# Optimization experiments

Measured on AMD Instinct MI355X. Metric: run time of the kernel, lower is better.

The kernel has to match this reference:

```python
import jax, jax.numpy as jnp
import numpy as np

B, T, M, DK, DV, S = 64, 256, 64, 128, 256, 128
NSK, NQ = 200, 2000


def _glorot(k, shape):
    lim = np.sqrt(6.0 / (shape[0] + shape[1])).astype(np.float32)
    return jax.random.uniform(k, shape, jnp.float32, -lim, lim)


def setup_inputs() -> dict:
    key = jax.random.key(0)
    ks = jax.random.split(key, 16)
    tn = lambda k, shape: 0.1 * jax.random.truncated_normal(k, -2.0, 2.0, shape, jnp.float32)
    return {
        "q_data": jax.random.randint(ks[0], (B, T), 0, NSK + 1),
        "qa_data": jax.random.randint(ks[1], (B, T), 0, 2 * NSK + 1),
        "s_data": jax.random.randint(ks[2], (B, T), 0, NQ + 1),
        "key_memory": tn(ks[3], (M, DK)),
        "value_memory": tn(ks[4], (M, DV)),
        "Eq": 0.05 * jax.random.normal(ks[5], (NSK + 1, DK), jnp.float32),
        "Eqa": 0.05 * jax.random.normal(ks[6], (2 * NSK + 1, DV), jnp.float32),
        "Es": 0.05 * jax.random.normal(ks[7], (NQ + 1, DK), jnp.float32),
        "We": _glorot(ks[8], (DV, DV)), "be": jnp.zeros((DV,), jnp.float32),
        "Wa": _glorot(ks[9], (DV, DV)), "ba": jnp.zeros((DV,), jnp.float32),
        "Wsa": _glorot(ks[10], (DV, M)), "bsa": jnp.zeros((M,), jnp.float32),
        "Wqd1": _glorot(ks[11], (DK, S)), "bqd1": jnp.zeros((S,), jnp.float32),
        "Wqd": _glorot(ks[12], (S, 1)), "bqd": jnp.zeros((1,), jnp.float32),
        "Wsd1": _glorot(ks[13], (DK, S)), "bsd1": jnp.zeros((S,), jnp.float32),
        "Wsd": _glorot(ks[14], (S, 1)), "bsd": jnp.zeros((1,), jnp.float32),
    }


def reference(q_data, qa_data, s_data, key_memory, value_memory, Eq, Eqa, Es,
              We, be, Wa, ba, Wsa, bsa, Wqd1, bqd1, Wqd, bqd, Wsd1, bsd1, Wsd, bsd):
    b = q_data.shape[0]
    qe = Eq[q_data]    # [B,T,DK]
    qae = Eqa[qa_data]  # [B,T,DV]
    se = Es[s_data]    # [B,T,DK]
    # time-independent precomputation (same math, hoisted out of the loop)
    corr = jax.nn.softmax(jnp.einsum("btk,mk->btm", qe, key_memory), axis=-1)  # [B,T,M]
    erase = qae @ We + be  # [B,T,DV] (activation=None in source)
    add = qae @ Wa + ba    # [B,T,DV]
    qd = jnp.tanh(qe @ Wqd1 + bqd1) @ Wqd + bqd  # [B,T,1]
    sd = jnp.tanh(se @ Wsd1 + bsd1) @ Wsd + bsd  # [B,T,1]

    def step(Mv, x):
        cw, er, ad = x  # [B,M], [B,DV], [B,DV]
        read = jnp.einsum("bm,bmd->bd", cw, Mv)        # read BEFORE write
        sa1 = read @ Wsa + bsa                          # [B,M]
        sa = jnp.sum(cw * sa1, axis=1)                  # [B]
        scale = cw[:, :, None]                          # [B,M,1]
        Mv_new = Mv * (1.0 - er[:, None, :] * scale) + ad[:, None, :] * scale
        return Mv_new, sa

    Mv0 = jnp.broadcast_to(value_memory[None], (b,) + value_memory.shape)
    xs = (corr.transpose(1, 0, 2), erase.transpose(1, 0, 2), add.transpose(1, 0, 2))
    _, sa_t = jax.lax.scan(step, Mv0, xs)  # sa_t: [T,B]
    z = 3.0 * sa_t.T - qd[..., 0] - sd[..., 0]  # [B,T]
    return jax.nn.sigmoid(z)
```

## Files before the change

### kernel.cpp

```cpp
#include <hip/hip_runtime.h>
#include <math.h>

#define B_   64
#define T_   256
#define M_   64
#define DK_  128
#define DV_  256
#define S_   128
#define NQR  201
#define NQAR 401
#define NSR  2001

static __device__ __forceinline__ int imin(int a, int b){ return a < b ? a : b; }

static __device__ __forceinline__ float fast_tanh(float x){
  float e = __expf(2.f * x);
  return 1.f - 2.f / (e + 1.f);
}

template<int CTRL, int RM>
static __device__ __forceinline__ float dppadd(float x) {
  return x + __int_as_float(
      __builtin_amdgcn_update_dpp(0, __float_as_int(x), CTRL, RM, 0xf, true));
}
static __device__ __forceinline__ float wave_sum_lane63(float x) {
  x = dppadd<0x111, 0xf>(x);
  x = dppadd<0x112, 0xf>(x);
  x = dppadd<0x114, 0xf>(x);
  x = dppadd<0x118, 0xf>(x);
  x = dppadd<0x142, 0xa>(x);
  x = dppadd<0x143, 0xc>(x);
  return x;
}

__device__ void corr_role(int blk, const float* __restrict__ Eq,
                          const float* __restrict__ Km,
                          const float* __restrict__ Wsa,
                          const float* __restrict__ bsa,
                          float* __restrict__ corr,
                          float* __restrict__ w2_t,
                          float* __restrict__ csb_t)
{
  __shared__ float eq[4][DK_];
  __shared__ float cwb[4][M_];
  const int w = threadIdx.x >> 6, m = threadIdx.x & 63;
  const int i  = blk * 4 + w;
  const int ic = imin(i, NQR - 1);
  eq[w][m]      = Eq[ic * DK_ + m];
  eq[w][m + 64] = Eq[ic * DK_ + 64 + m];
  float acc = 0.f;
  const float4* kr = (const float4*)(Km + m * DK_);
  #pragma unroll 8
  for (int k4 = 0; k4 < DK_ / 4; ++k4) {
    float4 kv = kr[k4];
    acc = fmaf(eq[w][k4 * 4 + 0], kv.x, acc);
    acc = fmaf(eq[w][k4 * 4 + 1], kv.y, acc);
    acc = fmaf(eq[w][k4 * 4 + 2], kv.z, acc);
    acc = fmaf(eq[w][k4 * 4 + 3], kv.w, acc);
  }
  float mx = acc;
  #pragma unroll
  for (int off = 32; off; off >>= 1) mx = fmaxf(mx, __shfl_xor(mx, off, 64));
  float e = __expf(acc - mx);
  float ssum = e;
  #pragma unroll
  for (int off = 32; off; off >>= 1) ssum += __shfl_xor(ssum, off, 64);
  const float cw = e / ssum;
  if (i < NQR) corr[i * M_ + m] = cw;
  cwb[w][m] = cw;

  float pv = wave_sum_lane63(cw * bsa[m]);
  if (m == 63 && i < NQR) csb_t[i] = pv;

  float aw[4] = {0,0,0,0};
  for (int mm = 0; mm < M_; ++mm) {
    const float c = cwb[w][mm];
    #pragma unroll
    for (int r = 0; r < 4; ++r)
      aw[r] = fmaf(c, Wsa[(r * 64 + m) * M_ + mm], aw[r]);
  }
  if (i < NQR) {
    #pragma unroll
    for (int r = 0; r < 4; ++r) w2_t[i * DV_ + r * 64 + m] = aw[r];
  }
}

__device__ void ea_role(int blk, const float* __restrict__ Eqa,
                        const float* __restrict__ We, const float* __restrict__ be,
                        const float* __restrict__ Wa, const float* __restrict__ ba,
                        float* __restrict__ ert, float* __restrict__ adt)
{
  __shared__ float a[8][DV_];
  const int d  = threadIdx.x;
  const int i0 = blk * 8;
  #pragma unroll
  for (int r = 0; r < 8; ++r) a[r][d] = Eqa[imin(i0 + r, NQAR - 1) * DV_ + d];
  __syncthreads();
  float er[8] = {0,0,0,0,0,0,0,0}, ad[8] = {0,0,0,0,0,0,0,0};
  for (int k = 0; k < DV_; ++k) {
    float we = We[k * DV_ + d];
    float wa = Wa[k * DV_ + d];
    #pragma unroll
    for (int r = 0; r < 8; ++r) {
      er[r] = fmaf(a[r][k], we, er[r]);
      ad[r] = fmaf(a[r][k], wa, ad[r]);
    }
  }
  const float beo = be[d], bao = ba[d];
  #pragma unroll
  for (int r = 0; r < 8; ++r) {
    int i = i0 + r;
    if (i < NQAR) { ert[i * DV_ + d] = er[r] + beo; adt[i * DV_ + d] = ad[r] + bao; }
  }
}

__device__ void mlp_role(int blk, const float* __restrict__ E,
                         const float* __restrict__ W1, const float* __restrict__ b1,
                         const float* __restrict__ W2v, const float* __restrict__ b2,
                         float* __restrict__ outt, int nrows)
{
  __shared__ float e[8 * S_];
  __shared__ float red[8][2];
  const int tid = threadIdx.x;
  const int s = tid & 127, rh = tid >> 7;
  const int i0 = blk * 8;
  #pragma unroll
  for (int j = 0; j < 4; ++j) {
    int x = tid + j * 256;
    int row = imin(i0 + (x >> 7), nrows - 1);
    e[x] = E[row * DK_ + (x & 127)];
  }
  __syncthreads();
  float acc[4] = {0,0,0,0};
  const float* eb = e + rh * 4 * 128;
  for (int k = 0; k < DK_; ++k) {
    float wv = W1[k * S_ + s];
    #pragma unroll
    for (int r = 0; r < 4; ++r) acc[r] = fmaf(eb[r * 128 + k], wv, acc[r]);
  }
  const float b1s = b1[s], w2s = W2v[s];
  float p[4];
  #pragma unroll
  for (int r = 0; r < 4; ++r) p[r] = fast_tanh(acc[r] + b1s) * w2s;
  #pragma unroll
  for (int r = 0; r < 4; ++r) p[r] = wave_sum_lane63(p[r]);
  const int lane = tid & 63;
  const int half = s >> 6;
  if (lane == 63) {
    #pragma unroll
    for (int r = 0; r < 4; ++r) red[rh * 4 + r][half] = p[r];
  }
  __syncthreads();
  if (tid < 8) {
    int i = i0 + tid;
    if (i < nrows) outt[i] = red[tid][0] + red[tid][1] + b2[0];
  }
}

#define NB_CORR 51
#define NB_EA   51
#define NB_QD   26
#define NB_SD   251
#define NB_TOT  (NB_CORR + NB_EA + NB_QD + NB_SD)

__global__ __launch_bounds__(256) void tables_kernel(
    const float* Eq, const float* Km, const float* Wsa, const float* bsa,
    float* corr_t, float* w2_t, float* csb_t,
    const float* Eqa, const float* We, const float* be,
    const float* Wa, const float* ba, float* er_t, float* ad_t,
    const float* Wqd1, const float* bqd1, const float* Wqd, const float* bqd, float* qd_t,
    const float* Es, const float* Wsd1, const float* bsd1, const float* Wsd, const float* bsd, float* sd_t)
{
  int blk = blockIdx.x;
  if (blk < NB_CORR) { corr_role(blk, Eq, Km, Wsa, bsa, corr_t, w2_t, csb_t); return; }
  blk -= NB_CORR;
  if (blk < NB_EA)   { ea_role(blk, Eqa, We, be, Wa, ba, er_t, ad_t); return; }
  blk -= NB_EA;
  if (blk < NB_QD)   { mlp_role(blk, Eq, Wqd1, bqd1, Wqd, bqd, qd_t, NQR); return; }
  blk -= NB_QD;
  mlp_role(blk, Es, Wsd1, bsd1, Wsd, bsd, sd_t, NSR);
}

struct SOps { float4 c; float er, ad, w2; };

static __device__ __forceinline__ void fetch4(
    int ii, const int4& qq, const int4& qaq, int m0, int d,
    const float* __restrict__ corr_t, const float* __restrict__ er_t,
    const float* __restrict__ ad_t, const float* __restrict__ w2_t,
    SOps (&o)[4])
{
  const int q0 = __builtin_amdgcn_readlane(qq.x,  ii);
  const int q1 = __builtin_amdgcn_readlane(qq.y,  ii);
  const int q2 = __builtin_amdgcn_readlane(qq.z,  ii);
  const int q3 = __builtin_amdgcn_readlane(qq.w,  ii);
  const int a0 = __builtin_amdgcn_readlane(qaq.x, ii);
  const int a1 = __builtin_amdgcn_readlane(qaq.y, ii);
  const int a2 = __builtin_amdgcn_readlane(qaq.z, ii);
  const int a3 = __builtin_amdgcn_readlane(qaq.w, ii);
  o[0].c = *(const float4*)(corr_t + q0 * M_ + m0);
  o[1].c = *(const float4*)(corr_t + q1 * M_ + m0);
  o[2].c = *(const float4*)(corr_t + q2 * M_ + m0);
  o[3].c = *(const float4*)(corr_t + q3 * M_ + m0);
  o[0].er = er_t[a0 * DV_ + d];  o[0].ad = ad_t[a0 * DV_ + d];  o[0].w2 = w2_t[q0 * DV_ + d];
  o[1].er = er_t[a1 * DV_ + d];  o[1].ad = ad_t[a1 * DV_ + d];  o[1].w2 = w2_t[q1 * DV_ + d];
  o[2].er = er_t[a2 * DV_ + d];  o[2].ad = ad_t[a2 * DV_ + d];  o[2].w2 = w2_t[q2 * DV_ + d];
  o[3].er = er_t[a3 * DV_ + d];  o[3].ad = ad_t[a3 * DV_ + d];  o[3].w2 = w2_t[q3 * DV_ + d];
}

static __device__ __forceinline__ float step1(float (&Mv)[4], const SOps& o)
{
  float r0 = Mv[0] * o.c.x;
  float r1 = Mv[1] * o.c.y;
  r0 = fmaf(Mv[2], o.c.z, r0);
  r1 = fmaf(Mv[3], o.c.w, r1);
  Mv[0] = fmaf(o.c.x, fmaf(-o.er, Mv[0], o.ad), Mv[0]);
  Mv[1] = fmaf(o.c.y, fmaf(-o.er, Mv[1], o.ad), Mv[1]);
  Mv[2] = fmaf(o.c.z, fmaf(-o.er, Mv[2], o.ad), Mv[2]);
  Mv[3] = fmaf(o.c.w, fmaf(-o.er, Mv[3], o.ad), Mv[3]);
  return wave_sum_lane63((r0 + r1) * o.w2);
}

__global__ __launch_bounds__(512) void scan_kernel(
    const int* __restrict__ q_data, const int* __restrict__ qa_data,
    const float* __restrict__ corr_t, const float* __restrict__ er_t,
    const float* __restrict__ ad_t, const float* __restrict__ w2_t,
    const float* __restrict__ Vm, float* __restrict__ sa_part)
{
  const int b  = blockIdx.y;
  const int xx = blockIdx.x;
  const int dq = xx >> 1;
  const int mh = xx & 1;
  const int tid = threadIdx.x;
  const int dl  = tid & 63;
  const int w   = tid >> 6;
  const int mg  = mh * 8 + w;
  const int m0  = __builtin_amdgcn_readfirstlane(mg * 4);
  const int d   = dq * 64 + dl;

  const int4 qq  = ((const int4*)(q_data  + b * T_))[dl];
  const int4 qaq = ((const int4*)(qa_data + b * T_))[dl];

  float Mv[4];
  #pragma unroll
  for (int j = 0; j < 4; ++j) Mv[j] = Vm[(m0 + j) * DV_ + d];

  float* baseP = sa_part + ((dq * 16 + mg) * B_ + b) * T_;

  SOps A[4], B[4];
  fetch4(0, qq, qaq, m0, d, corr_t, er_t, ad_t, w2_t, A);
  fetch4(1, qq, qaq, m0, d, corr_t, er_t, ad_t, w2_t, B);

  for (int i = 0; i < 64; i += 2) {
    float4 pA;
    pA.x = step1(Mv, A[0]);
    pA.y = step1(Mv, A[1]);
    pA.z = step1(Mv, A[2]);
    pA.w = step1(Mv, A[3]);
    fetch4((i + 2) & 63, qq, qaq, m0, d, corr_t, er_t, ad_t, w2_t, A);
    if (dl == 63) *(float4*)(baseP + 4 * i) = pA;

    float4 pB;
    pB.x = step1(Mv, B[0]);
    pB.y = step1(Mv, B[1]);
    pB.z = step1(Mv, B[2]);
    pB.w = step1(Mv, B[3]);
    fetch4((i + 3) & 63, qq, qaq, m0, d, corr_t, er_t, ad_t, w2_t, B);
    if (dl == 63) *(float4*)(baseP + 4 * i + 4) = pB;
  }
}

__global__ __launch_bounds__(256) void final_kernel(
    const int* __restrict__ q_data, const int* __restrict__ s_data,
    const float* __restrict__ sa_part, const float* __restrict__ csb_t,
    const float* __restrict__ qd_t, const float* __restrict__ sd_t,
    float* __restrict__ out)
{
  const int b = blockIdx.x, t = threadIdx.x;
  float s = 0.f;
  #pragma unroll
  for (int p = 0; p < 64; ++p) s += sa_part[(p * B_ + b) * T_ + t];
  const int bt = b * T_ + t;
  const int q  = q_data[bt];
  const int si = s_data[bt];
  const float sa = s + csb_t[q];
  const float z = 3.f * sa - qd_t[q] - sd_t[si];
  out[bt] = 1.f / (1.f + __expf(-z));
}

extern "C" void kernel_launch(void* const* d_in, const int* in_sizes, int n_in,
                              void* d_out, int out_size, void* d_ws, size_t ws_size,
                              hipStream_t stream)
{
  const int*   q_data = (const int*)d_in[0];
  const int*   qa_data= (const int*)d_in[1];
  const int*   s_data = (const int*)d_in[2];
  const float* Km     = (const float*)d_in[3];
  const float* Vm     = (const float*)d_in[4];
  const float* Eq     = (const float*)d_in[5];
  const float* Eqa    = (const float*)d_in[6];
  const float* Es     = (const float*)d_in[7];
  const float* We     = (const float*)d_in[8];
  const float* be     = (const float*)d_in[9];
  const float* Wa     = (const float*)d_in[10];
  const float* ba     = (const float*)d_in[11];
  const float* Wsa    = (const float*)d_in[12];
  const float* bsa    = (const float*)d_in[13];
  const float* Wqd1   = (const float*)d_in[14];
  const float* bqd1   = (const float*)d_in[15];
  const float* Wqd    = (const float*)d_in[16];
  const float* bqd    = (const float*)d_in[17];
  const float* Wsd1   = (const float*)d_in[18];
  const float* bsd1   = (const float*)d_in[19];
  const float* Wsd    = (const float*)d_in[20];
  const float* bsd    = (const float*)d_in[21];
  float* out = (float*)d_out;

  float* wsf    = (float*)d_ws;
  float* corr_t = wsf;
  float* w2_t   = corr_t + NQR * M_;
  float* csb_t  = w2_t + NQR * DV_;
  float* er_t   = csb_t + 204;
  float* ad_t   = er_t + NQAR * DV_;
  float* qd_t   = ad_t + NQAR * DV_;
  float* sd_t   = qd_t + 204;
  float* sa_p   = sd_t + 2004;

  tables_kernel<<<NB_TOT, 256, 0, stream>>>(
      Eq, Km, Wsa, bsa, corr_t, w2_t, csb_t,
      Eqa, We, be, Wa, ba, er_t, ad_t,
      Wqd1, bqd1, Wqd, bqd, qd_t,
      Es, Wsd1, bsd1, Wsd, bsd, sd_t);
  scan_kernel<<<dim3(8, B_), 512, 0, stream>>>(q_data, qa_data, corr_t, er_t, ad_t, w2_t, Vm, sa_p);
  final_kernel<<<B_, 256, 0, stream>>>(q_data, s_data, sa_p, csb_t, qd_t, sd_t, out);
}
```

Before: 195.4 us.

## Give each scan thread eight memory rows instead of four, halving scan blocks

Each scan wave now owns 8 memory slots per value column instead of 4. The grid shrinks from 8x64 to 4x64 blocks, and the final kernel reduces 32 partial sums instead of 64. This amortizes the per-step er/ad/w2 gathers and the cross-wave reduction (wave_sum) over twice the state, so fewer redundant loads and reductions happen per unit of work. The cost is fewer blocks, 256 instead of 512, on a 256-CU device, which lowers parallelism. Each thread also carries more registers and does more serial work per step.

```diff
diff --git a/kernel.cpp b/kernel.cpp
--- a/kernel.cpp
+++ b/kernel.cpp
@@ -181,42 +181,51 @@
   mlp_role(blk, Es, Wsd1, bsd1, Wsd, bsd, sd_t, NSR);
 }
 
-struct SOps { float4 c; float er, ad, w2; };
-
-static __device__ __forceinline__ void fetch4(
-    int ii, const int4& qq, const int4& qaq, int m0, int d,
+struct SOps { float er, ad, w2; };
+
+static __device__ __forceinline__ void fetchg(
+    int g, const int4& qq, const int4& qaq, int m0, int d,
     const float* __restrict__ corr_t, const float* __restrict__ er_t,
     const float* __restrict__ ad_t, const float* __restrict__ w2_t,
-    SOps (&o)[4])
-{
-  const int q0 = __builtin_amdgcn_readlane(qq.x,  ii);
-  const int q1 = __builtin_amdgcn_readlane(qq.y,  ii);
-  const int q2 = __builtin_amdgcn_readlane(qq.z,  ii);
-  const int q3 = __builtin_amdgcn_readlane(qq.w,  ii);
-  const int a0 = __builtin_amdgcn_readlane(qaq.x, ii);
-  const int a1 = __builtin_amdgcn_readlane(qaq.y, ii);
-  const int a2 = __builtin_amdgcn_readlane(qaq.z, ii);
-  const int a3 = __builtin_amdgcn_readlane(qaq.w, ii);
-  o[0].c = *(const float4*)(corr_t + q0 * M_ + m0);
-  o[1].c = *(const float4*)(corr_t + q1 * M_ + m0);
-  o[2].c = *(const float4*)(corr_t + q2 * M_ + m0);
-  o[3].c = *(const float4*)(corr_t + q3 * M_ + m0);
+    float4 (&cA)[4], float4 (&cB)[4], SOps (&o)[4])
+{
+  const int q0 = __builtin_amdgcn_readlane(qq.x,  g);
+  const int q1 = __builtin_amdgcn_readlane(qq.y,  g);
+  const int q2 = __builtin_amdgcn_readlane(qq.z,  g);
+  const int q3 = __builtin_amdgcn_readlane(qq.w,  g);
+  const int a0 = __builtin_amdgcn_readlane(qaq.x, g);
+  const int a1 = __builtin_amdgcn_readlane(qaq.y, g);
+  const int a2 = __builtin_amdgcn_readlane(qaq.z, g);
+  const int a3 = __builtin_amdgcn_readlane(qaq.w, g);
+  cA[0] = *(const float4*)(corr_t + q0 * M_ + m0);
+  cB[0] = *(const float4*)(corr_t + q0 * M_ + m0 + 4);
+  cA[1] = *(const float4*)(corr_t + q1 * M_ + m0);
+  cB[1] = *(const float4*)(corr_t + q1 * M_ + m0 + 4);
+  cA[2] = *(const float4*)(corr_t + q2 * M_ + m0);
+  cB[2] = *(const float4*)(corr_t + q2 * M_ + m0 + 4);
+  cA[3] = *(const float4*)(corr_t + q3 * M_ + m0);
+  cB[3] = *(const float4*)(corr_t + q3 * M_ + m0 + 4);
   o[0].er = er_t[a0 * DV_ + d];  o[0].ad = ad_t[a0 * DV_ + d];  o[0].w2 = w2_t[q0 * DV_ + d];
   o[1].er = er_t[a1 * DV_ + d];  o[1].ad = ad_t[a1 * DV_ + d];  o[1].w2 = w2_t[q1 * DV_ + d];
   o[2].er = er_t[a2 * DV_ + d];  o[2].ad = ad_t[a2 * DV_ + d];  o[2].w2 = w2_t[q2 * DV_ + d];
   o[3].er = er_t[a3 * DV_ + d];  o[3].ad = ad_t[a3 * DV_ + d];  o[3].w2 = w2_t[q3 * DV_ + d];
 }
 
-static __device__ __forceinline__ float step1(float (&Mv)[4], const SOps& o)
-{
-  float r0 = Mv[0] * o.c.x;
-  float r1 = Mv[1] * o.c.y;
-  r0 = fmaf(Mv[2], o.c.z, r0);
-  r1 = fmaf(Mv[3], o.c.w, r1);
-  Mv[0] = fmaf(o.c.x, fmaf(-o.er, Mv[0], o.ad), Mv[0]);
-  Mv[1] = fmaf(o.c.y, fmaf(-o.er, Mv[1], o.ad), Mv[1]);
-  Mv[2] = fmaf(o.c.z, fmaf(-o.er, Mv[2], o.ad), Mv[2]);
-  Mv[3] = fmaf(o.c.w, fmaf(-o.er, Mv[3], o.ad), Mv[3]);
+static __device__ __forceinline__ float stepf(
+    float (&Mv)[8], const float4& ca, const float4& cb, const SOps& o)
+{
+  const float c[8] = {ca.x, ca.y, ca.z, ca.w, cb.x, cb.y, cb.z, cb.w};
+  float r0 = c[0] * Mv[0];
+  float r1 = c[1] * Mv[1];
+  #pragma unroll
+  for (int j = 0; j < 8; ++j) {
+    if (j >= 2) {
+      if (j & 1) r1 = fmaf(c[j], Mv[j], r1);
+      else       r0 = fmaf(c[j], Mv[j], r0);
+    }
+    const float tmp = fmaf(-o.er, Mv[j], o.ad);
+    Mv[j] = fmaf(c[j], tmp, Mv[j]);
+  }
   return wave_sum_lane63((r0 + r1) * o.w2);
 }
 
@@ -226,46 +235,44 @@
     const float* __restrict__ ad_t, const float* __restrict__ w2_t,
     const float* __restrict__ Vm, float* __restrict__ sa_part)
 {
-  const int b  = blockIdx.y;
-  const int xx = blockIdx.x;
-  const int dq = xx >> 1;
-  const int mh = xx & 1;
+  const int b   = blockIdx.y;
+  const int dq  = blockIdx.x;
   const int tid = threadIdx.x;
   const int dl  = tid & 63;
   const int w   = tid >> 6;
-  const int mg  = mh * 8 + w;
-  const int m0  = __builtin_amdgcn_readfirstlane(mg * 4);
+  const int m0  = __builtin_amdgcn_readfirstlane(w * 8);
   const int d   = dq * 64 + dl;
 
   const int4 qq  = ((const int4*)(q_data  + b * T_))[dl];
   const int4 qaq = ((const int4*)(qa_data + b * T_))[dl];
 
-  float Mv[4];
-  #pragma unroll
-  for (int j = 0; j < 4; ++j) Mv[j] = Vm[(m0 + j) * DV_ + d];
-
-  float* baseP = sa_part + ((dq * 16 + mg) * B_ + b) * T_;
-
-  SOps A[4], B[4];
-  fetch4(0, qq, qaq, m0, d, corr_t, er_t, ad_t, w2_t, A);
-  fetch4(1, qq, qaq, m0, d, corr_t, er_t, ad_t, w2_t, B);
-
-  for (int i = 0; i < 64; i += 2) {
+  float Mv[8];
+  #pragma unroll
+  for (int j = 0; j < 8; ++j) Mv[j] = Vm[(m0 + j) * DV_ + d];
+
+  float* baseP = sa_part + ((dq * 8 + w) * B_ + b) * T_;
+
+  float4 cAA[4], cBA[4], cAB[4], cBB[4];
+  SOps oA[4], oB[4];
+  fetchg(0, qq, qaq, m0, d, corr_t, er_t, ad_t, w2_t, cAA, cBA, oA);
+  fetchg(1, qq, qaq, m0, d, corr_t, er_t, ad_t, w2_t, cAB, cBB, oB);
+
+  for (int g = 0; g < 64; g += 2) {
     float4 pA;
-    pA.x = step1(Mv, A[0]);
-    pA.y = step1(Mv, A[1]);
-    pA.z = step1(Mv, A[2]);
-    pA.w = step1(Mv, A[3]);
-    fetch4((i + 2) & 63, qq, qaq, m0, d, corr_t, er_t, ad_t, w2_t, A);
-    if (dl == 63) *(float4*)(baseP + 4 * i) = pA;
+    pA.x = stepf(Mv, cAA[0], cBA[0], oA[0]);
+    pA.y = stepf(Mv, cAA[1], cBA[1], oA[1]);
+    pA.z = stepf(Mv, cAA[2], cBA[2], oA[2]);
+    pA.w = stepf(Mv, cAA[3], cBA[3], oA[3]);
+    fetchg((g + 2) & 63, qq, qaq, m0, d, corr_t, er_t, ad_t, w2_t, cAA, cBA, oA);
+    if (dl == 63) *(float4*)(baseP + 4 * g) = pA;
 
     float4 pB;
-    pB.x = step1(Mv, B[0]);
-    pB.y = step1(Mv, B[1]);
-    pB.z = step1(Mv, B[2]);
-    pB.w = step1(Mv, B[3]);
-    fetch4((i + 3) & 63, qq, qaq, m0, d, corr_t, er_t, ad_t, w2_t, B);
-    if (dl == 63) *(float4*)(baseP + 4 * i + 4) = pB;
+    pB.x = stepf(Mv, cAB[0], cBB[0], oB[0]);
+    pB.y = stepf(Mv, cAB[1], cBB[1], oB[1]);
+    pB.z = stepf(Mv, cAB[2], cBB[2], oB[2]);
+    pB.w = stepf(Mv, cAB[3], cBB[3], oB[3]);
+    fetchg((g + 3) & 63, qq, qaq, m0, d, corr_t, er_t, ad_t, w2_t, cAB, cBB, oB);
+    if (dl == 63) *(float4*)(baseP + 4 * g + 4) = pB;
   }
 }
 
@@ -278,7 +285,7 @@
   const int b = blockIdx.x, t = threadIdx.x;
   float s = 0.f;
   #pragma unroll
-  for (int p = 0; p < 64; ++p) s += sa_part[(p * B_ + b) * T_ + t];
+  for (int p = 0; p < 32; ++p) s += sa_part[(p * B_ + b) * T_ + t];
   const int bt = b * T_ + t;
   const int q  = q_data[bt];
   const int si = s_data[bt];
@@ -330,6 +337,6 @@
       Eqa, We, be, Wa, ba, er_t, ad_t,
       Wqd1, bqd1, Wqd, bqd, qd_t,
       Es, Wsd1, bsd1, Wsd, bsd, sd_t);
-  scan_kernel<<<dim3(8, B_), 512, 0, stream>>>(q_data, qa_data, corr_t, er_t, ad_t, w2_t, Vm, sa_p);
+  scan_kernel<<<dim3(4, B_), 512, 0, stream>>>(q_data, qa_data, corr_t, er_t, ad_t, w2_t, Vm, sa_p);
   final_kernel<<<B_, 256, 0, stream>>>(q_data, s_data, sa_p, csb_t, qd_t, sd_t, out);
 }
```

Measured after the change: 173.6 us. 11.2% less time.
